# Performance work log

Hardware: AMD Instinct MI355X
Metric: run time of the kernel (lower is better)

## Reference

```python
import jax, jax.numpy as jnp
import numpy as np
from functools import partial

N_USERS = 100000
N_ITEMS = 50000
EMB = 64
N_FACTORS = 4
N_ITER = 2
N_LAYERS = 2
E = 2000000
EPS = 1e-12  # F.normalize eps


def setup_inputs() -> dict:
    key = jax.random.key(0)
    k1, k2, k3, k4 = jax.random.split(key, 4)
    N = N_USERS + N_ITEMS
    user_emb = jax.random.normal(k1, (N_USERS, EMB), jnp.float32) * 0.1
    item_emb = jax.random.normal(k2, (N_ITEMS, EMB), jnp.float32) * 0.1
    # first N entries cover every node once so row/col degree sums are > 0
    # (original norm_adj has no isolated nodes; avoids 1/sqrt(0))
    h = jnp.concatenate([jnp.arange(N, dtype=jnp.int32),
                         jax.random.randint(k3, (E - N,), 0, N, jnp.int32)])
    t = jnp.concatenate([jnp.arange(N, dtype=jnp.int32)[::-1],
                         jax.random.randint(k4, (E - N,), 0, N, jnp.int32)])
    return {"user_emb": user_emb, "item_emb": item_emb, "h_list": h, "t_list": t}


def _l2norm(x):
    n = jnp.sqrt(jnp.sum(x * x, axis=-1, keepdims=True))
    return x / jnp.maximum(n, EPS)


def _dgcf_embed(user_emb, item_emb, h_list, t_list):
    N = user_emb.shape[0] + item_emb.shape[0]
    d = user_emb.shape[1]
    F = N_FACTORS
    df = d // F
    Ee = h_list.shape[0]
    seg = partial(jax.ops.segment_sum, num_segments=N)
    seg_h = jax.vmap(lambda v: seg(v, h_list))  # batched over factor axis

    ego = jnp.concatenate([user_emb, item_emb], 0)  # [N, d]
    all_embeds = [ego]
    A_values = jnp.ones((F, Ee), ego.dtype)  # routing logits, persist across layers

    for _ in range(N_LAYERS):
        x = ego.reshape(N, F, df).transpose(1, 0, 2)  # [F, N, df] factor chunks
        out = x
        for _ in range(N_ITER):
            scores = jax.nn.softmax(A_values, axis=0)        # [F, E]
            rowsum = seg_h(scores)                           # [F, N] sparse.sum(A, dim=1)
            d_col = 1.0 / jnp.sqrt(rowsum)                   # [F, N]
            # out = D_col @ A @ D_col @ x  (original uses D_col on both sides)
            y = d_col[:, :, None] * x                        # [F, N, df]
            msg = scores[:, :, None] * y[:, t_list, :]       # [F, E, df]
            out = d_col[:, :, None] * seg_h(msg)             # [F, N, df]
            # routing score update: cosine-ish affinity head(new) vs tanh(tail(old))
            head = _l2norm(out[:, h_list, :])                # [F, E, df]
            tail = _l2norm(x[:, t_list, :])                  # [F, E, df]
            A_values = A_values + jnp.sum(head * jnp.tanh(tail), axis=-1)
        ego = out.transpose(1, 0, 2).reshape(N, d)           # concat factor outputs
        all_embeds.append(ego)

    all_emb = jnp.mean(jnp.stack(all_embeds, 1), axis=1)     # [N, d]
    return all_emb[:user_emb.shape[0]], all_emb[user_emb.shape[0]:]


def reference(user_emb, item_emb, h_list, t_list):
    return _dgcf_embed(user_emb, item_emb, h_list, t_list)
```

## Files before the change

kernel.cpp:

```cpp
#include <hip/hip_runtime.h>
#include <hip/hip_bf16.h>

#define DEMB 64
typedef unsigned short u16;
typedef _Float16 f16;
typedef _Float16 f16x2 __attribute__((ext_vector_type(2)));
typedef float f32x2 __attribute__((ext_vector_type(2)));

#if defined(__has_builtin)
#if __has_builtin(__builtin_amdgcn_fdot2)
#define USE_FDOT2 1
#endif
#endif

__device__ __forceinline__ u16 f2h(float f) {
    union { f16 h; u16 u; } c; c.h = (f16)f; return c.u;
}

__device__ __forceinline__ float ptanh5(float a) {
    float a2 = a * a;
    float t = fmaf(a2, -0.030095f, 0.124066f);
    t = fmaf(a2, t, -0.332377f);
    t = fmaf(a2, t, 1.0f);
    return a * t;
}

__global__ void init_A_kernel(float4* __restrict__ A, int E) {
    int e = blockIdx.x * blockDim.x + threadIdx.x;
    if (e < E) A[e] = make_float4(1.f, 1.f, 1.f, 1.f);
}

__global__ void concat_copy_kernel(const float* __restrict__ u, const float* __restrict__ it,
                                   float* __restrict__ x, float* __restrict__ acc,
                                   int nu_elems, int total) {
    int i = blockIdx.x * blockDim.x + threadIdx.x;
    if (i >= total) return;
    float v = (i < nu_elems) ? u[i] : it[i - nu_elems];
    x[i] = v;
    acc[i] = v;
}

__global__ void hist_kernel(const int* __restrict__ h, int* __restrict__ ghist,
                            int E, int EPB, int NB) {
    __shared__ int bins[1024];
    int b = blockIdx.x, tid = threadIdx.x;
    for (int j = tid; j < NB; j += 256) bins[j] = 0;
    __syncthreads();
    int s = b * EPB, e = min(s + EPB, E);
    for (int k = s + tid; k < e; k += 256)
        atomicAdd(&bins[((unsigned)h[k]) >> 8], 1);
    __syncthreads();
    for (int j = tid; j < NB; j += 256) ghist[j * gridDim.x + b] = bins[j];
}

__global__ void btot_kernel(const int* __restrict__ ghist, int* __restrict__ btot) {
    __shared__ int s[256];
    int j = blockIdx.x, tid = threadIdx.x;
    s[tid] = ghist[j * 256 + tid];
    __syncthreads();
    for (int o = 128; o >= 1; o >>= 1) {
        if (tid < o) s[tid] += s[tid + o];
        __syncthreads();
    }
    if (tid == 0) btot[j] = s[0];
}

__global__ void bscan_kernel(const int* __restrict__ btot, int* __restrict__ bbase,
                             int NB, int E) {
    __shared__ int s[1024];
    int tid = threadIdx.x;
    int v = (tid < NB) ? btot[tid] : 0;
    s[tid] = v;
    __syncthreads();
    for (int o = 1; o < 1024; o <<= 1) {
        int a = (tid >= o) ? s[tid - o] : 0;
        __syncthreads();
        s[tid] += a;
        __syncthreads();
    }
    if (tid < NB) bbase[tid] = s[tid] - v;
    if (tid == 0) bbase[NB] = E;
}

__global__ void bofs_kernel(int* __restrict__ ghist, const int* __restrict__ bbase) {
    __shared__ int s[256];
    int j = blockIdx.x, tid = threadIdx.x;
    int v = ghist[j * 256 + tid];
    s[tid] = v;
    __syncthreads();
    for (int o = 1; o < 256; o <<= 1) {
        int a = (tid >= o) ? s[tid - o] : 0;
        __syncthreads();
        s[tid] += a;
        __syncthreads();
    }
    ghist[j * 256 + tid] = bbase[j] + s[tid] - v;
}

__global__ void scatter_kernel(const int* __restrict__ h, const int* __restrict__ t,
                               const int* __restrict__ ghist, unsigned* __restrict__ stg,
                               int E, int EPB, int NB) {
    __shared__ int cur[1024];
    int b = blockIdx.x, tid = threadIdx.x;
    for (int j = tid; j < NB; j += 256) cur[j] = ghist[j * gridDim.x + b];
    __syncthreads();
    int s = b * EPB, e = min(s + EPB, E);
    for (int k = s + tid; k < e; k += 256) {
        unsigned hh = (unsigned)h[k];
        int pos = atomicAdd(&cur[hh >> 8], 1);
        stg[pos] = ((hh & 255u) << 18) | (unsigned)t[k];
    }
}

__global__ void finalize_kernel(const unsigned* __restrict__ stg, const int* __restrict__ bbase,
                                int* __restrict__ off, int* __restrict__ csr_t, int N, int E) {
    __shared__ int cnt[256];
    __shared__ int scn[256];
    int b = blockIdx.x, tid = threadIdx.x;
    int ebeg = bbase[b], eend = bbase[b + 1];
    cnt[tid] = 0;
    __syncthreads();
    for (int k = ebeg + tid; k < eend; k += 256)
        atomicAdd(&cnt[(stg[k] >> 18) & 255u], 1);
    __syncthreads();
    int v = cnt[tid];
    scn[tid] = v;
    __syncthreads();
    for (int o = 1; o < 256; o <<= 1) {
        int a = (tid >= o) ? scn[tid - o] : 0;
        __syncthreads();
        scn[tid] += a;
        __syncthreads();
    }
    int excl = scn[tid] - v;
    int gn = (b << 8) + tid;
    if (gn < N) off[gn] = ebeg + excl;
    if (b == 0 && tid == 0) off[N] = E;
    __syncthreads();
    cnt[tid] = excl;
    __syncthreads();
    for (int k = ebeg + tid; k < eend; k += 256) {
        unsigned en = stg[k];
        int slot = atomicAdd(&cnt[(en >> 18) & 255u], 1);
        csr_t[ebeg + slot] = (int)(en & 0x3FFFFu);
    }
}

__global__ void dcol0_kernel(const int* __restrict__ off, float* __restrict__ dcol, int N) {
    int n = blockIdx.x * blockDim.x + threadIdx.x;
    if (n >= N) return;
    float v = 0.5f * rsqrtf((float)(off[n + 1] - off[n]));
    *(float4*)(dcol + (size_t)n * 4) = make_float4(v, v, v, v);
}

__global__ void prep_kernel(const float* __restrict__ x, u16* __restrict__ xs,
                            u16* __restrict__ tailt, int total) {
    int i = blockIdx.x * blockDim.x + threadIdx.x;
    if (i >= total) return;
    float v = x[i];
    xs[i] = f2h(v);
    float s = v * v;
#pragma unroll
    for (int o = 8; o >= 1; o >>= 1) s += __shfl_xor(s, o);
    float nr = fmaxf(sqrtf(s), 1e-12f);
    tailt[i] = f2h(ptanh5(v * __builtin_amdgcn_rcpf(nr)));
}

template <bool UNI, bool WOUT, bool ROUTE, int ACC>
__global__ void message_kernel(const int* __restrict__ off, const int* __restrict__ csr_t,
                               float* __restrict__ Acsr, float* __restrict__ prob,
                               const u16* __restrict__ xs, const u16* __restrict__ tailt,
                               const float* __restrict__ dcol_in, float* __restrict__ dcol_out,
                               float* __restrict__ out, float* __restrict__ acc, int N) {
    int gid = blockIdx.x * blockDim.x + threadIdx.x;
    int n = gid >> 6;
    if (n >= N) return;
    int l = gid & 63;
    int g = l >> 3;
    int m = l & 7;
    unsigned f = (unsigned)(m >> 1);
    int s = off[n], e = off[n + 1];
    unsigned moff = (unsigned)(m << 3);

    union U8 { uint4 u; f16 h[8]; f16x2 p[4]; };

    float a0 = 0.f, a1 = 0.f, a2 = 0.f, a3 = 0.f;
    float a4 = 0.f, a5 = 0.f, a6 = 0.f, a7 = 0.f;

#pragma unroll 2
    for (int k = s; k < e; k += 16) {
        int e1 = k + g, e2 = e1 + 8;
        bool v1 = e1 < e, v2 = e2 < e;
        unsigned c1 = (unsigned)(v1 ? e1 : s);
        unsigned c2 = (unsigned)(v2 ? e2 : s);
        unsigned t1 = (unsigned)csr_t[c1];
        unsigned t2 = (unsigned)csr_t[c2];
        float p1, p2;
        if (UNI) {
            p1 = dcol_in[t1 * 4u + f];
            p2 = dcol_in[t2 * 4u + f];
        } else {
            p1 = prob[c1 * 4u + f] * dcol_in[t1 * 4u + f];
            p2 = prob[c2 * 4u + f] * dcol_in[t2 * 4u + f];
        }
        p1 = v1 ? p1 : 0.f;
        p2 = v2 ? p2 : 0.f;
        U8 w1, w2;
        w1.u = *(const uint4*)(xs + (t1 << 6) + moff);
        w2.u = *(const uint4*)(xs + (t2 << 6) + moff);
        a0 = fmaf(p1, (float)w1.h[0], a0); a1 = fmaf(p1, (float)w1.h[1], a1);
        a2 = fmaf(p1, (float)w1.h[2], a2); a3 = fmaf(p1, (float)w1.h[3], a3);
        a4 = fmaf(p1, (float)w1.h[4], a4); a5 = fmaf(p1, (float)w1.h[5], a5);
        a6 = fmaf(p1, (float)w1.h[6], a6); a7 = fmaf(p1, (float)w1.h[7], a7);
        a0 = fmaf(p2, (float)w2.h[0], a0); a1 = fmaf(p2, (float)w2.h[1], a1);
        a2 = fmaf(p2, (float)w2.h[2], a2); a3 = fmaf(p2, (float)w2.h[3], a3);
        a4 = fmaf(p2, (float)w2.h[4], a4); a5 = fmaf(p2, (float)w2.h[5], a5);
        a6 = fmaf(p2, (float)w2.h[6], a6); a7 = fmaf(p2, (float)w2.h[7], a7);
    }

#pragma unroll
    for (int o = 8; o <= 32; o <<= 1) {
        a0 += __shfl_xor(a0, o); a1 += __shfl_xor(a1, o);
        a2 += __shfl_xor(a2, o); a3 += __shfl_xor(a3, o);
        a4 += __shfl_xor(a4, o); a5 += __shfl_xor(a5, o);
        a6 += __shfl_xor(a6, o); a7 += __shfl_xor(a7, o);
    }

    if (WOUT || ACC != 0) {
        float dn = dcol_in[(unsigned)n * 4u + f];
        if (l < 8) {
            unsigned oidx = ((unsigned)n << 6) + moff;
            float4 lo = make_float4(a0 * dn, a1 * dn, a2 * dn, a3 * dn);
            float4 hi = make_float4(a4 * dn, a5 * dn, a6 * dn, a7 * dn);
            if (WOUT) {
                *(float4*)(out + oidx) = lo;
                *(float4*)(out + oidx + 4) = hi;
            }
            if (ACC == 1) {
                float4 c0 = *(const float4*)(acc + oidx);
                float4 c1 = *(const float4*)(acc + oidx + 4);
                *(float4*)(acc + oidx) =
                    make_float4(c0.x + lo.x, c0.y + lo.y, c0.z + lo.z, c0.w + lo.w);
                *(float4*)(acc + oidx + 4) =
                    make_float4(c1.x + hi.x, c1.y + hi.y, c1.z + hi.z, c1.w + hi.w);
            } else if (ACC == 2) {
                const float k3 = 1.0f / 3.0f;
                float4 c0 = *(const float4*)(acc + oidx);
                float4 c1 = *(const float4*)(acc + oidx + 4);
                *(float4*)(acc + oidx) =
                    make_float4((c0.x + lo.x) * k3, (c0.y + lo.y) * k3,
                                (c0.z + lo.z) * k3, (c0.w + lo.w) * k3);
                *(float4*)(acc + oidx + 4) =
                    make_float4((c1.x + hi.x) * k3, (c1.y + hi.y) * k3,
                                (c1.z + hi.z) * k3, (c1.w + hi.w) * k3);
            }
        }
    }
    if (!ROUTE) return;

    float ss = a0 * a0 + a1 * a1 + a2 * a2 + a3 * a3
             + a4 * a4 + a5 * a5 + a6 * a6 + a7 * a7;
    ss += __shfl_xor(ss, 1);
    float inv = 1.0f / fmaxf(sqrtf(ss), 1e-12f);
    float h0 = a0 * inv, h1 = a1 * inv, h2 = a2 * inv, h3 = a3 * inv;
    float h4 = a4 * inv, h5 = a5 * inv, h6 = a6 * inv, h7 = a7 * inv;
#ifdef USE_FDOT2
    f16x2 hp0 = {(f16)h0, (f16)h1};
    f16x2 hp1 = {(f16)h2, (f16)h3};
    f16x2 hp2 = {(f16)h4, (f16)h5};
    f16x2 hp3 = {(f16)h6, (f16)h7};
#endif

    float rowsumf = 0.f;

#pragma unroll 2
    for (int k = s; k < e; k += 16) {
        int e1 = k + g, e2 = e1 + 8;
        bool v1 = e1 < e, v2 = e2 < e;
        unsigned c1 = (unsigned)(v1 ? e1 : s);
        unsigned c2 = (unsigned)(v2 ? e2 : s);
        unsigned t1 = (unsigned)csr_t[c1];
        unsigned t2 = (unsigned)csr_t[c2];
        U8 u1, u2;
        u1.u = *(const uint4*)(tailt + (t1 << 6) + moff);
        u2.u = *(const uint4*)(tailt + (t2 << 6) + moff);
        float d1, d2;
#ifdef USE_FDOT2
        d1 = __builtin_amdgcn_fdot2(hp0, u1.p[0], 0.f, false);
        d1 = __builtin_amdgcn_fdot2(hp1, u1.p[1], d1, false);
        d1 = __builtin_amdgcn_fdot2(hp2, u1.p[2], d1, false);
        d1 = __builtin_amdgcn_fdot2(hp3, u1.p[3], d1, false);
        d2 = __builtin_amdgcn_fdot2(hp0, u2.p[0], 0.f, false);
        d2 = __builtin_amdgcn_fdot2(hp1, u2.p[1], d2, false);
        d2 = __builtin_amdgcn_fdot2(hp2, u2.p[2], d2, false);
        d2 = __builtin_amdgcn_fdot2(hp3, u2.p[3], d2, false);
#else
        d1 = h0 * (float)u1.h[0] + h1 * (float)u1.h[1]
           + h2 * (float)u1.h[2] + h3 * (float)u1.h[3]
           + h4 * (float)u1.h[4] + h5 * (float)u1.h[5]
           + h6 * (float)u1.h[6] + h7 * (float)u1.h[7];
        d2 = h0 * (float)u2.h[0] + h1 * (float)u2.h[1]
           + h2 * (float)u2.h[2] + h3 * (float)u2.h[3]
           + h4 * (float)u2.h[4] + h5 * (float)u2.h[5]
           + h6 * (float)u2.h[6] + h7 * (float)u2.h[7];
#endif
        d1 += __shfl_xor(d1, 1);
        d2 += __shfl_xor(d2, 1);
        unsigned ai1 = c1 * 4u + f;
        unsigned ai2 = c2 * 4u + f;
        float na1 = Acsr[ai1] + d1;
        float na2 = Acsr[ai2] + d2;
        float ex1 = __expf(na1);
        float ex2 = __expf(na2);
        float se1 = ex1 + __shfl_xor(ex1, 2); se1 += __shfl_xor(se1, 4);
        float se2 = ex2 + __shfl_xor(ex2, 2); se2 += __shfl_xor(se2, 4);
        float p1 = ex1 * __builtin_amdgcn_rcpf(se1);
        float p2 = ex2 * __builtin_amdgcn_rcpf(se2);
        if ((m & 1) == 0) {
            if (v1) { Acsr[ai1] = na1; prob[ai1] = p1; }
            if (v2) { Acsr[ai2] = na2; prob[ai2] = p2; }
        }
        rowsumf += (v1 ? p1 : 0.f) + (v2 ? p2 : 0.f);
    }

    rowsumf += __shfl_xor(rowsumf, 8);
    rowsumf += __shfl_xor(rowsumf, 16);
    rowsumf += __shfl_xor(rowsumf, 32);
    if (l < 8 && (m & 1) == 0) dcol_out[(unsigned)n * 4u + f] = rsqrtf(rowsumf);
}

extern "C" void kernel_launch(void* const* d_in, const int* in_sizes, int n_in,
                              void* d_out, int out_size, void* d_ws, size_t ws_size,
                              hipStream_t stream) {
    const float* user_emb = (const float*)d_in[0];
    const float* item_emb = (const float*)d_in[1];
    const int* h = (const int*)d_in[2];
    const int* t = (const int*)d_in[3];

    const int nu_elems = in_sizes[0];
    const int ni_elems = in_sizes[1];
    const int total = nu_elems + ni_elems;
    const int N = total / DEMB;
    const int E = in_sizes[2];
    const int NB = (N + 255) >> 8;
    const int NBLK = 256;
    const int EPB = (E + NBLK - 1) / NBLK;

    float* acc = (float*)d_out;

    float* x     = (float*)d_ws;
    float* out   = x + (size_t)total;
    float* Acsr  = out + (size_t)total;
    float* prob  = Acsr + (size_t)4 * E;
    float* dcolA = prob + (size_t)4 * E;
    float* dcolB = dcolA + (size_t)4 * N;
    u16* xs      = (u16*)(dcolB + (size_t)4 * N);
    u16* tailt   = xs + (size_t)total;
    int* ghist   = (int*)(tailt + (size_t)total);
    int* btot    = ghist + (size_t)NB * 256;
    int* bbase   = btot + ((NB + 3) & ~3);
    int* off     = bbase + ((NB + 5) & ~3);
    int* csr_t   = off + ((N + 4) & ~3);
    unsigned* stg = (unsigned*)prob;

    const int BLK = 256;
    const int gE = (E + BLK - 1) / BLK;
    const int gTot = (total + BLK - 1) / BLK;
    const int gN = (N + BLK - 1) / BLK;
    const int gNodeWave = (N * 64 + BLK - 1) / BLK;

    concat_copy_kernel<<<gTot, BLK, 0, stream>>>(user_emb, item_emb, x, acc, nu_elems, total);

    hist_kernel<<<NBLK, 256, 0, stream>>>(h, ghist, E, EPB, NB);
    btot_kernel<<<NB, 256, 0, stream>>>(ghist, btot);
    bscan_kernel<<<1, 1024, 0, stream>>>(btot, bbase, NB, E);
    bofs_kernel<<<NB, 256, 0, stream>>>(ghist, bbase);
    scatter_kernel<<<NBLK, 256, 0, stream>>>(h, t, ghist, stg, E, EPB, NB);
    finalize_kernel<<<NB, 256, 0, stream>>>(stg, bbase, off, csr_t, N, E);

    init_A_kernel<<<gE, BLK, 0, stream>>>((float4*)Acsr, E);
    dcol0_kernel<<<gN, BLK, 0, stream>>>(off, dcolA, N);

    prep_kernel<<<gTot, BLK, 0, stream>>>(x, xs, tailt, total);
    message_kernel<true, false, true, 0><<<gNodeWave, BLK, 0, stream>>>(
        off, csr_t, Acsr, prob, xs, tailt, dcolA, dcolB, out, acc, N);
    message_kernel<false, true, true, 1><<<gNodeWave, BLK, 0, stream>>>(
        off, csr_t, Acsr, prob, xs, tailt, dcolB, dcolA, out, acc, N);

    prep_kernel<<<gTot, BLK, 0, stream>>>(out, xs, tailt, total);
    message_kernel<false, false, true, 0><<<gNodeWave, BLK, 0, stream>>>(
        off, csr_t, Acsr, prob, xs, tailt, dcolA, dcolB, x, acc, N);
    message_kernel<false, false, false, 2><<<gNodeWave, BLK, 0, stream>>>(
        off, csr_t, Acsr, prob, xs, tailt, dcolB, dcolA, x, acc, N);
}
```

Measured before the change: 573.5 us.

## Drop precomputed tanh tail table; recompute tanh from fp16 x with per-factor inverse norms

Removes the separate fp16 tanh(normalized x) table. The routing pass now gathers the same fp16 x rows plus a per-node, per-factor inverse norm and evaluates the polynomial tanh inline. The first 16-edge chunk of gathered x rows is cached in shared memory so the routing pass can reuse it without a second global gather. This cuts gather traffic and table writes, but adds ALU work: eight polynomial evaluations per lane per edge replace the packed fp16 dot instructions.

Measured after the change: 547.5 us. 4.5% less time.

```diff
diff --git a/kernel.cpp b/kernel.cpp
--- a/kernel.cpp
+++ b/kernel.cpp
@@ -4,14 +4,6 @@
 #define DEMB 64
 typedef unsigned short u16;
 typedef _Float16 f16;
-typedef _Float16 f16x2 __attribute__((ext_vector_type(2)));
-typedef float f32x2 __attribute__((ext_vector_type(2)));
-
-#if defined(__has_builtin)
-#if __has_builtin(__builtin_amdgcn_fdot2)
-#define USE_FDOT2 1
-#endif
-#endif
 
 __device__ __forceinline__ u16 f2h(float f) {
     union { f16 h; u16 u; } c; c.h = (f16)f; return c.u;
@@ -154,7 +146,7 @@
 }
 
 __global__ void prep_kernel(const float* __restrict__ x, u16* __restrict__ xs,
-                            u16* __restrict__ tailt, int total) {
+                            float* __restrict__ invnx, int total) {
     int i = blockIdx.x * blockDim.x + threadIdx.x;
     if (i >= total) return;
     float v = x[i];
@@ -162,33 +154,69 @@
     float s = v * v;
 #pragma unroll
     for (int o = 8; o >= 1; o >>= 1) s += __shfl_xor(s, o);
-    float nr = fmaxf(sqrtf(s), 1e-12f);
-    tailt[i] = f2h(ptanh5(v * __builtin_amdgcn_rcpf(nr)));
+    if ((i & 15) == 0) invnx[i >> 4] = 1.0f / fmaxf(sqrtf(s), 1e-12f);
 }
 
 template <bool UNI, bool WOUT, bool ROUTE, int ACC>
 __global__ void message_kernel(const int* __restrict__ off, const int* __restrict__ csr_t,
                                float* __restrict__ Acsr, float* __restrict__ prob,
-                               const u16* __restrict__ xs, const u16* __restrict__ tailt,
+                               const u16* __restrict__ xs, const float* __restrict__ invnx,
                                const float* __restrict__ dcol_in, float* __restrict__ dcol_out,
                                float* __restrict__ out, float* __restrict__ acc, int N) {
+    __shared__ uint4 cache[4][16][8];
     int gid = blockIdx.x * blockDim.x + threadIdx.x;
     int n = gid >> 6;
     if (n >= N) return;
-    int l = gid & 63;
+    int tid = threadIdx.x;
+    int wid = tid >> 6;
+    int l = tid & 63;
     int g = l >> 3;
     int m = l & 7;
     unsigned f = (unsigned)(m >> 1);
     int s = off[n], e = off[n + 1];
     unsigned moff = (unsigned)(m << 3);
 
-    union U8 { uint4 u; f16 h[8]; f16x2 p[4]; };
+    union U8 { uint4 u; f16 h[8]; };
 
     float a0 = 0.f, a1 = 0.f, a2 = 0.f, a3 = 0.f;
     float a4 = 0.f, a5 = 0.f, a6 = 0.f, a7 = 0.f;
 
-#pragma unroll 2
-    for (int k = s; k < e; k += 16) {
+    auto accum = [&](const U8& w1, const U8& w2, float p1, float p2) {
+        a0 = fmaf(p1, (float)w1.h[0], a0); a1 = fmaf(p1, (float)w1.h[1], a1);
+        a2 = fmaf(p1, (float)w1.h[2], a2); a3 = fmaf(p1, (float)w1.h[3], a3);
+        a4 = fmaf(p1, (float)w1.h[4], a4); a5 = fmaf(p1, (float)w1.h[5], a5);
+        a6 = fmaf(p1, (float)w1.h[6], a6); a7 = fmaf(p1, (float)w1.h[7], a7);
+        a0 = fmaf(p2, (float)w2.h[0], a0); a1 = fmaf(p2, (float)w2.h[1], a1);
+        a2 = fmaf(p2, (float)w2.h[2], a2); a3 = fmaf(p2, (float)w2.h[3], a3);
+        a4 = fmaf(p2, (float)w2.h[4], a4); a5 = fmaf(p2, (float)w2.h[5], a5);
+        a6 = fmaf(p2, (float)w2.h[6], a6); a7 = fmaf(p2, (float)w2.h[7], a7);
+    };
+
+    {
+        int e1 = s + g, e2 = e1 + 8;
+        bool v1 = e1 < e, v2 = e2 < e;
+        unsigned c1 = (unsigned)(v1 ? e1 : s);
+        unsigned c2 = (unsigned)(v2 ? e2 : s);
+        unsigned t1 = (unsigned)csr_t[c1];
+        unsigned t2 = (unsigned)csr_t[c2];
+        float p1, p2;
+        if (UNI) {
+            p1 = dcol_in[t1 * 4u + f];
+            p2 = dcol_in[t2 * 4u + f];
+        } else {
+            p1 = prob[c1 * 4u + f] * dcol_in[t1 * 4u + f];
+            p2 = prob[c2 * 4u + f] * dcol_in[t2 * 4u + f];
+        }
+        p1 = v1 ? p1 : 0.f;
+        p2 = v2 ? p2 : 0.f;
+        U8 w1, w2;
+        w1.u = *(const uint4*)(xs + (t1 << 6) + moff);
+        w2.u = *(const uint4*)(xs + (t2 << 6) + moff);
+        cache[wid][g][m] = w1.u;
+        cache[wid][g + 8][m] = w2.u;
+        accum(w1, w2, p1, p2);
+    }
+    for (int k = s + 16; k < e; k += 16) {
         int e1 = k + g, e2 = e1 + 8;
         bool v1 = e1 < e, v2 = e2 < e;
         unsigned c1 = (unsigned)(v1 ? e1 : s);
@@ -208,14 +236,7 @@
         U8 w1, w2;
         w1.u = *(const uint4*)(xs + (t1 << 6) + moff);
         w2.u = *(const uint4*)(xs + (t2 << 6) + moff);
-        a0 = fmaf(p1, (float)w1.h[0], a0); a1 = fmaf(p1, (float)w1.h[1], a1);
-        a2 = fmaf(p1, (float)w1.h[2], a2); a3 = fmaf(p1, (float)w1.h[3], a3);
-        a4 = fmaf(p1, (float)w1.h[4], a4); a5 = fmaf(p1, (float)w1.h[5], a5);
-        a6 = fmaf(p1, (float)w1.h[6], a6); a7 = fmaf(p1, (float)w1.h[7], a7);
-        a0 = fmaf(p2, (float)w2.h[0], a0); a1 = fmaf(p2, (float)w2.h[1], a1);
-        a2 = fmaf(p2, (float)w2.h[2], a2); a3 = fmaf(p2, (float)w2.h[3], a3);
-        a4 = fmaf(p2, (float)w2.h[4], a4); a5 = fmaf(p2, (float)w2.h[5], a5);
-        a6 = fmaf(p2, (float)w2.h[6], a6); a7 = fmaf(p2, (float)w2.h[7], a7);
+        accum(w1, w2, p1, p2);
     }
 
 #pragma unroll
@@ -262,48 +283,30 @@
              + a4 * a4 + a5 * a5 + a6 * a6 + a7 * a7;
     ss += __shfl_xor(ss, 1);
     float inv = 1.0f / fmaxf(sqrtf(ss), 1e-12f);
-    float h0 = a0 * inv, h1 = a1 * inv, h2 = a2 * inv, h3 = a3 * inv;
-    float h4 = a4 * inv, h5 = a5 * inv, h6 = a6 * inv, h7 = a7 * inv;
-#ifdef USE_FDOT2
-    f16x2 hp0 = {(f16)h0, (f16)h1};
-    f16x2 hp1 = {(f16)h2, (f16)h3};
-    f16x2 hp2 = {(f16)h4, (f16)h5};
-    f16x2 hp3 = {(f16)h6, (f16)h7};
-#endif
+    float hv[8];
+    hv[0] = a0 * inv; hv[1] = a1 * inv; hv[2] = a2 * inv; hv[3] = a3 * inv;
+    hv[4] = a4 * inv; hv[5] = a5 * inv; hv[6] = a6 * inv; hv[7] = a7 * inv;
+
+    auto tdot = [&](const U8& w, float iv) -> float {
+        float d = 0.f;
+#pragma unroll
+        for (int i = 0; i < 8; ++i)
+            d = fmaf(hv[i], ptanh5((float)w.h[i] * iv), d);
+        return d;
+    };
 
     float rowsumf = 0.f;
 
-#pragma unroll 2
-    for (int k = s; k < e; k += 16) {
-        int e1 = k + g, e2 = e1 + 8;
+    auto route = [&](int kbase, const U8& w1, const U8& w2,
+                     unsigned t1, unsigned t2) {
+        int e1 = kbase + g, e2 = e1 + 8;
         bool v1 = e1 < e, v2 = e2 < e;
         unsigned c1 = (unsigned)(v1 ? e1 : s);
         unsigned c2 = (unsigned)(v2 ? e2 : s);
-        unsigned t1 = (unsigned)csr_t[c1];
-        unsigned t2 = (unsigned)csr_t[c2];
-        U8 u1, u2;
-        u1.u = *(const uint4*)(tailt + (t1 << 6) + moff);
-        u2.u = *(const uint4*)(tailt + (t2 << 6) + moff);
-        float d1, d2;
-#ifdef USE_FDOT2
-        d1 = __builtin_amdgcn_fdot2(hp0, u1.p[0], 0.f, false);
-        d1 = __builtin_amdgcn_fdot2(hp1, u1.p[1], d1, false);
-        d1 = __builtin_amdgcn_fdot2(hp2, u1.p[2], d1, false);
-        d1 = __builtin_amdgcn_fdot2(hp3, u1.p[3], d1, false);
-        d2 = __builtin_amdgcn_fdot2(hp0, u2.p[0], 0.f, false);
-        d2 = __builtin_amdgcn_fdot2(hp1, u2.p[1], d2, false);
-        d2 = __builtin_amdgcn_fdot2(hp2, u2.p[2], d2, false);
-        d2 = __builtin_amdgcn_fdot2(hp3, u2.p[3], d2, false);
-#else
-        d1 = h0 * (float)u1.h[0] + h1 * (float)u1.h[1]
-           + h2 * (float)u1.h[2] + h3 * (float)u1.h[3]
-           + h4 * (float)u1.h[4] + h5 * (float)u1.h[5]
-           + h6 * (float)u1.h[6] + h7 * (float)u1.h[7];
-        d2 = h0 * (float)u2.h[0] + h1 * (float)u2.h[1]
-           + h2 * (float)u2.h[2] + h3 * (float)u2.h[3]
-           + h4 * (float)u2.h[4] + h5 * (float)u2.h[5]
-           + h6 * (float)u2.h[6] + h7 * (float)u2.h[7];
-#endif
+        float iv1 = invnx[t1 * 4u + f];
+        float iv2 = invnx[t2 * 4u + f];
+        float d1 = tdot(w1, iv1);
+        float d2 = tdot(w2, iv2);
         d1 += __shfl_xor(d1, 1);
         d2 += __shfl_xor(d2, 1);
         unsigned ai1 = c1 * 4u + f;
@@ -321,6 +324,29 @@
             if (v2) { Acsr[ai2] = na2; prob[ai2] = p2; }
         }
         rowsumf += (v1 ? p1 : 0.f) + (v2 ? p2 : 0.f);
+    };
+
+    {
+        int e1 = s + g, e2 = e1 + 8;
+        unsigned c1 = (unsigned)((e1 < e) ? e1 : s);
+        unsigned c2 = (unsigned)((e2 < e) ? e2 : s);
+        unsigned t1 = (unsigned)csr_t[c1];
+        unsigned t2 = (unsigned)csr_t[c2];
+        U8 w1, w2;
+        w1.u = cache[wid][g][m];
+        w2.u = cache[wid][g + 8][m];
+        route(s, w1, w2, t1, t2);
+    }
+    for (int k = s + 16; k < e; k += 16) {
+        int e1 = k + g, e2 = e1 + 8;
+        unsigned c1 = (unsigned)((e1 < e) ? e1 : s);
+        unsigned c2 = (unsigned)((e2 < e) ? e2 : s);
+        unsigned t1 = (unsigned)csr_t[c1];
+        unsigned t2 = (unsigned)csr_t[c2];
+        U8 w1, w2;
+        w1.u = *(const uint4*)(xs + (t1 << 6) + moff);
+        w2.u = *(const uint4*)(xs + (t2 << 6) + moff);
+        route(k, w1, w2, t1, t2);
     }
 
     rowsumf += __shfl_xor(rowsumf, 8);
@@ -354,9 +380,9 @@
     float* prob  = Acsr + (size_t)4 * E;
     float* dcolA = prob + (size_t)4 * E;
     float* dcolB = dcolA + (size_t)4 * N;
-    u16* xs      = (u16*)(dcolB + (size_t)4 * N);
-    u16* tailt   = xs + (size_t)total;
-    int* ghist   = (int*)(tailt + (size_t)total);
+    float* invnx = dcolB + (size_t)4 * N;
+    u16* xs      = (u16*)(invnx + (size_t)4 * N);
+    int* ghist   = (int*)(xs + (size_t)total);
     int* btot    = ghist + (size_t)NB * 256;
     int* bbase   = btot + ((NB + 3) & ~3);
     int* off     = bbase + ((NB + 5) & ~3);
@@ -381,15 +407,15 @@
     init_A_kernel<<<gE, BLK, 0, stream>>>((float4*)Acsr, E);
     dcol0_kernel<<<gN, BLK, 0, stream>>>(off, dcolA, N);
 
-    prep_kernel<<<gTot, BLK, 0, stream>>>(x, xs, tailt, total);
+    prep_kernel<<<gTot, BLK, 0, stream>>>(x, xs, invnx, total);
     message_kernel<true, false, true, 0><<<gNodeWave, BLK, 0, stream>>>(
-        off, csr_t, Acsr, prob, xs, tailt, dcolA, dcolB, out, acc, N);
+        off, csr_t, Acsr, prob, xs, invnx, dcolA, dcolB, out, acc, N);
     message_kernel<false, true, true, 1><<<gNodeWave, BLK, 0, stream>>>(
-        off, csr_t, Acsr, prob, xs, tailt, dcolB, dcolA, out, acc, N);
-
-    prep_kernel<<<gTot, BLK, 0, stream>>>(out, xs, tailt, total);
+        off, csr_t, Acsr, prob, xs, invnx, dcolB, dcolA, out, acc, N);
+
+    prep_kernel<<<gTot, BLK, 0, stream>>>(out, xs, invnx, total);
     message_kernel<false, false, true, 0><<<gNodeWave, BLK, 0, stream>>>(
-        off, csr_t, Acsr, prob, xs, tailt, dcolA, dcolB, x, acc, N);
+        off, csr_t, Acsr, prob, xs, invnx, dcolA, dcolB, x, acc, N);
     message_kernel<false, false, false, 2><<<gNodeWave, BLK, 0, stream>>>(
-        off, csr_t, Acsr, prob, xs, tailt, dcolB, dcolA, x, acc, N);
-}
+        off, csr_t, Acsr, prob, xs, invnx, dcolB, dcolA, x, acc, N);
+}
```
